# Kernel tuning notes

Hardware: AMD Instinct MI355X
Metric: run time of the kernel (lower is better)

The kernel has to match this reference:

```python
import jax, jax.numpy as jnp
import numpy as np

WS = 7           # window size
NH = 12          # num heads
EPS_ADA = 1e-6   # AdaLayerNorm eps
EPS_LN = 1e-5    # torch nn.LayerNorm default eps


def _rel_pos_index(ws):
    coords = np.stack(np.meshgrid(np.arange(ws), np.arange(ws), indexing='ij'))  # (2,ws,ws)
    flat = coords.reshape(2, -1)                      # (2, N)
    rel = flat[:, :, None] - flat[:, None, :]         # (2, N, N)
    rel = rel.transpose(1, 2, 0).astype(np.int64)     # (N, N, 2)
    rel[:, :, 0] += ws - 1
    rel[:, :, 1] += ws - 1
    rel[:, :, 0] *= 2 * ws - 1
    return jnp.asarray(rel.sum(-1))                   # (N, N) in [0, (2ws-1)^2)

REL_IDX = _rel_pos_index(WS)


def setup_inputs() -> dict:
    key = jax.random.key(0)
    ks = jax.random.split(key, 8)
    B, H, W, C, COND = 32, 56, 56, 384, 128
    L = H * W
    s = 0.02
    return {
        'x_tok': jax.random.normal(ks[0], (B, L, C), jnp.float32),
        'z_tok': jax.random.normal(ks[1], (B, L, C), jnp.float32),
        'cond': jax.random.normal(ks[2], (B, COND), jnp.float32),
        'gamma_x': jnp.ones((C,), jnp.float32),
        'beta_x': jnp.zeros((C,), jnp.float32),
        'mod_w': jax.random.normal(ks[3], (COND, 2 * C), jnp.float32) * s,
        'mod_b': jnp.zeros((2 * C,), jnp.float32),
        'gamma_z': jnp.ones((C,), jnp.float32),
        'beta_z': jnp.zeros((C,), jnp.float32),
        'rel_bias_table': jax.random.normal(ks[4], ((2 * WS - 1) ** 2, NH), jnp.float32) * s,
        'q_w': jax.random.normal(ks[5], (C, C), jnp.float32) * s,
        'q_b': jnp.zeros((C,), jnp.float32),
        'kv_w': jax.random.normal(ks[6], (C, 2 * C), jnp.float32) * s,
        'kv_b': jnp.zeros((2 * C,), jnp.float32),
        'proj_w': jax.random.normal(ks[7], (C, C), jnp.float32) * s,
        'proj_b': jnp.zeros((C,), jnp.float32),
        'H': H,
        'W': W,
    }


def reference(x_tok, z_tok, cond, gamma_x, beta_x, mod_w, mod_b,
              gamma_z, beta_z, rel_bias_table, q_w, q_b, kv_w, kv_b,
              proj_w, proj_b, H, W):
    B, L, C = x_tok.shape
    hd = C // NH
    N = WS * WS

    # AdaLayerNorm-Zero on x
    mu = x_tok.mean(-1, keepdims=True)
    var = ((x_tok - mu) ** 2).mean(-1, keepdims=True)
    x_hat = (x_tok - mu) * jax.lax.rsqrt(var + EPS_ADA)
    mod = (cond @ mod_w + mod_b).reshape(B, 2, C)
    d_gamma, d_beta = mod[:, 0], mod[:, 1]
    x = (gamma_x * (1.0 + d_gamma))[:, None, :] * x_hat + (beta_x + d_beta)[:, None, :]

    # LayerNorm on z
    mz = z_tok.mean(-1, keepdims=True)
    vz = ((z_tok - mz) ** 2).mean(-1, keepdims=True)
    z = (z_tok - mz) * jax.lax.rsqrt(vz + EPS_LN) * gamma_z + beta_z

    # window partition: (B,H,W,C) -> (B*nW, N, C)
    def part(t):
        t = t.reshape(B, H // WS, WS, W // WS, WS, C)
        return t.transpose(0, 1, 3, 2, 4, 5).reshape(-1, N, C)

    x_win = part(x.reshape(B, H, W, C))
    z_win = part(z.reshape(B, H, W, C))

    # cross window attention
    q = (x_win @ q_w + q_b).reshape(-1, N, NH, hd).transpose(0, 2, 1, 3)  # (Bw,H,N,d)
    kv = (z_win @ kv_w + kv_b).reshape(-1, N, 2, NH, hd)
    k = kv[:, :, 0].transpose(0, 2, 1, 3)
    v = kv[:, :, 1].transpose(0, 2, 1, 3)
    scale = hd ** -0.5
    attn = jnp.einsum('bhnd,bhmd->bhnm', q * scale, k)                    # (Bw,H,N,N)
    bias = rel_bias_table[REL_IDX.reshape(-1)].reshape(N, N, NH).transpose(2, 0, 1)
    attn = jax.nn.softmax(attn + bias[None], axis=-1)
    out = jnp.einsum('bhnm,bhmd->bhnd', attn, v).transpose(0, 2, 1, 3).reshape(-1, N, C)
    out = out @ proj_w + proj_b

    # window reverse: (B*nW, N, C) -> (B, L, C)
    fused = out.reshape(B, H // WS, W // WS, WS, WS, C)
    fused = fused.transpose(0, 1, 3, 2, 4, 5).reshape(B, L, C)

    return x_tok + fused
```

## Files before the change

kernel.cpp:

```cpp
#include <hip/hip_runtime.h>
#include <hip/hip_bf16.h>

typedef float f32x4 __attribute__((ext_vector_type(4)));
typedef short short8 __attribute__((ext_vector_type(8)));
typedef __hip_bfloat16 bf16;

constexpr int CDIM  = 384;
constexpr int LTOK  = 3136;
constexpr int NWIN  = 2048;
constexpr int MROWS = 100352;
constexpr int MPAD  = MROWS + 64;

__device__ __forceinline__ void gload_lds16(const void* g, void* l) {
  __builtin_amdgcn_global_load_lds(
      (const __attribute__((address_space(1))) void*)g,
      (__attribute__((address_space(3))) void*)l, 16, 0, 0);
}

__device__ __forceinline__ void row_to_bl(int r, int& b, int& l) {
  int w = r / 49, n = r % 49;
  b = w >> 6;
  int wrem = w & 63;
  int wy = wrem >> 3, wx = wrem & 7;
  int ny = n / 7, nx = n % 7;
  l = (wy * 7 + ny) * 56 + wx * 7 + nx;
}


__global__ __launch_bounds__(256) void mod_kernel(
    const float* __restrict__ cond, const float* __restrict__ mw,
    const float* __restrict__ mb, float* __restrict__ mod) {
  int idx = blockIdx.x * 256 + threadIdx.x;
  int b = idx / 768, j = idx % 768;
  float s = mb[j];
  const float* cr = cond + b * 128;
  #pragma unroll 4
  for (int k = 0; k < 128; k++) s += cr[k] * mw[(size_t)k * 768 + j];
  mod[idx] = s;
}

__global__ __launch_bounds__(256) void prep_wt(
    const float* __restrict__ qw, const float* __restrict__ kvw,
    const float* __restrict__ pw,
    bf16* __restrict__ wtq, bf16* __restrict__ wtkv, bf16* __restrict__ wtp) {
  int idx = blockIdx.x * 256 + threadIdx.x;
  if (idx < 147456) {
    int n = idx / 384, k = idx % 384;
    wtq[idx] = __float2bfloat16(qw[(size_t)k * 384 + n]);
  } else if (idx < 147456 + 294912) {
    int i = idx - 147456;
    int n = i / 384, k = i % 384;
    wtkv[i] = __float2bfloat16(kvw[(size_t)k * 768 + n]);
  } else {
    int i = idx - 442368;
    int n = i / 384, k = i % 384;
    wtp[i] = __float2bfloat16(pw[(size_t)k * 384 + n]);
  }
}

__global__ __launch_bounds__(256) void bias_kernel(
    const float* __restrict__ tab, float* __restrict__ bT) {
  int idx = blockIdx.x * 256 + threadIdx.x;
  int h = idx >> 12, rem = idx & 4095, m = rem >> 6, c = rem & 63;
  float v;
  if (c >= 49)      v = -1e30f;
  else if (m >= 49) v = 0.f;
  else {
    int yq = m / 7, xq = m % 7, yk = c / 7, xk = c % 7;
    v = tab[((yq - yk + 6) * 13 + (xq - xk + 6)) * 12 + h];
  }
  bT[idx] = v;
}


__global__ __launch_bounds__(256) void ln_kernel(
    const float* __restrict__ src, const float* __restrict__ gamma,
    const float* __restrict__ beta, const float* __restrict__ mod,
    float eps, bf16* __restrict__ dst) {
  int wid = threadIdx.x >> 6, lane = threadIdx.x & 63;
  int r = blockIdx.x * 4 + wid;
  int bb, ll; row_to_bl(r, bb, ll);
  const float* x = src + ((size_t)bb * LTOK + ll) * 384;
  float v[6]; float s = 0.f, s2 = 0.f;
  #pragma unroll
  for (int i = 0; i < 6; i++) {
    v[i] = x[lane + 64 * i];
    s += v[i]; s2 += v[i] * v[i];
  }
  #pragma unroll
  for (int d = 1; d < 64; d <<= 1) { s += __shfl_xor(s, d); s2 += __shfl_xor(s2, d); }
  float mu = s * (1.f / 384.f);
  float var = s2 * (1.f / 384.f) - mu * mu;
  float rstd = rsqrtf(var + eps);
  bf16* o = dst + (size_t)r * 384;
  if (mod != nullptr) {
    const float* mg = mod + bb * 768;
    #pragma unroll
    for (int i = 0; i < 6; i++) {
      int c = lane + 64 * i;
      float y = (gamma[c] * (1.f + mg[c])) * ((v[i] - mu) * rstd) + beta[c] + mg[384 + c];
      o[c] = __float2bfloat16(y);
    }
  } else {
    #pragma unroll
    for (int i = 0; i < 6; i++) {
      int c = lane + 64 * i;
      o[c] = __float2bfloat16((v[i] - mu) * rstd * gamma[c] + beta[c]);
    }
  }
}


template<int MODE>
__global__ __launch_bounds__(256) void gemm_kernel(
    const bf16* __restrict__ A, const bf16* __restrict__ WT,
    const float* __restrict__ bias, void* __restrict__ outp,
    const float* __restrict__ resid, float scale, int N) {
  __shared__ __align__(16) bf16 As[128 * 64];
  __shared__ __align__(16) bf16 Bs[128 * 64];
  const int bm = blockIdx.x * 128;
  const int bn = blockIdx.y * 128;
  const int t = threadIdx.x;
  const int wid = t >> 6, lane = t & 63;
  const int r16 = lane & 15, g = lane >> 4;
  const int wr = wid >> 1, wc = wid & 1;

  f32x4 acc[4][4] = {};

  for (int k0 = 0; k0 < 384; k0 += 64) {
    if (k0) __syncthreads();
    #pragma unroll
    for (int i = 0; i < 4; i++) {
      int c = wid * 256 + i * 64 + lane;
      int row = c >> 3, col8 = (c & 7) << 3;
      gload_lds16(A + (size_t)(bm + row) * 384 + k0 + col8,
                  (char*)As + (size_t)(wid * 256 + i * 64) * 16);
    }
    #pragma unroll
    for (int i = 0; i < 4; i++) {
      int c = wid * 256 + i * 64 + lane;
      int row = c >> 3, col8 = (c & 7) << 3;
      gload_lds16(WT + (size_t)(bn + row) * 384 + k0 + col8,
                  (char*)Bs + (size_t)(wid * 256 + i * 64) * 16);
    }
    __syncthreads();
    #pragma unroll
    for (int kk = 0; kk < 2; kk++) {
      short8 a[4], b[4];
      #pragma unroll
      for (int m = 0; m < 4; m++)
        a[m] = *(const short8*)((const char*)As + (wr * 64 + m * 16 + r16) * 128 + kk * 64 + g * 16);
      #pragma unroll
      for (int n = 0; n < 4; n++)
        b[n] = *(const short8*)((const char*)Bs + (wc * 64 + n * 16 + r16) * 128 + kk * 64 + g * 16);
      #pragma unroll
      for (int m = 0; m < 4; m++)
        #pragma unroll
        for (int n = 0; n < 4; n++)
          acc[m][n] = __builtin_amdgcn_mfma_f32_16x16x32_bf16(a[m], b[n], acc[m][n], 0, 0, 0);
    }
  }

  if (MODE == 0) {
    bf16* O = (bf16*)outp;
    #pragma unroll
    for (int n = 0; n < 4; n++) {
      int col = bn + wc * 64 + n * 16 + r16;
      float bc = bias[col];
      #pragma unroll
      for (int m = 0; m < 4; m++) {
        int row0 = bm + wr * 64 + m * 16 + g * 4;
        #pragma unroll
        for (int r = 0; r < 4; r++) {
          float v = (acc[m][n][r] + bc) * scale;
          O[(size_t)(row0 + r) * N + col] = __float2bfloat16(v);
        }
      }
    }
  } else {
    float* O = (float*)outp;
    #pragma unroll
    for (int m = 0; m < 4; m++) {
      #pragma unroll
      for (int r = 0; r < 4; r++) {
        int row = bm + wr * 64 + m * 16 + g * 4 + r;
        int bb, ll; row_to_bl(row, bb, ll);
        size_t base = ((size_t)bb * LTOK + ll) * 384;
        #pragma unroll
        for (int n = 0; n < 4; n++) {
          int col = bn + wc * 64 + n * 16 + r16;
          O[base + col] = resid[base + col] + acc[m][n][r] + bias[col];
        }
      }
    }
  }
}


__global__ __launch_bounds__(64) void attn_kernel(
    const bf16* __restrict__ q, const bf16* __restrict__ kv,
    const float* __restrict__ biasT, bf16* __restrict__ o) {
  __shared__ __align__(16) bf16 vt[32][72];
  __shared__ __align__(16) bf16 P[64][72];
  const int h = blockIdx.x, w = blockIdx.y;
  const int lane = threadIdx.x;
  const int r16 = lane & 15, g = lane >> 4;
  const size_t qbase = (size_t)w * 49 * 384 + h * 32;
  const size_t kvbase = (size_t)w * 49 * 768 + h * 32;

  for (int e = lane; e < 32 * 72; e += 64) ((bf16*)vt)[e] = __float2bfloat16(0.f);
  for (int e = lane; e < 49 * 32; e += 64) {
    int c = e >> 5, d = e & 31;
    vt[d][c] = kv[kvbase + (size_t)c * 768 + 384 + d];
  }

  short8 aq[4], bk[4];
  #pragma unroll
  for (int mi = 0; mi < 4; mi++)
    aq[mi] = *(const short8*)(q + qbase + (size_t)(mi * 16 + r16) * 384 + g * 8);
  #pragma unroll
  for (int ni = 0; ni < 4; ni++)
    bk[ni] = *(const short8*)(kv + kvbase + (size_t)(ni * 16 + r16) * 768 + g * 8);

  f32x4 zero = {0.f, 0.f, 0.f, 0.f};
  f32x4 S[4][4];
  #pragma unroll
  for (int mi = 0; mi < 4; mi++)
    #pragma unroll
    for (int ni = 0; ni < 4; ni++)
      S[mi][ni] = __builtin_amdgcn_mfma_f32_16x16x32_bf16(aq[mi], bk[ni], zero, 0, 0, 0);

  const float* bt = biasT + h * 4096;
  #pragma unroll
  for (int mi = 0; mi < 4; mi++) {
    #pragma unroll
    for (int r = 0; r < 4; r++) {
      int rowm = mi * 16 + g * 4 + r;
      float sv[4];
      #pragma unroll
      for (int ni = 0; ni < 4; ni++)
        sv[ni] = S[mi][ni][r] + bt[rowm * 64 + ni * 16 + r16];
      float mx = fmaxf(fmaxf(sv[0], sv[1]), fmaxf(sv[2], sv[3]));
      #pragma unroll
      for (int d = 1; d < 16; d <<= 1) mx = fmaxf(mx, __shfl_xor(mx, d));
      float sum = 0.f;
      #pragma unroll
      for (int ni = 0; ni < 4; ni++) { sv[ni] = __expf(sv[ni] - mx); sum += sv[ni]; }
      #pragma unroll
      for (int d = 1; d < 16; d <<= 1) sum += __shfl_xor(sum, d);
      float inv = __fdividef(1.f, sum);
      #pragma unroll
      for (int ni = 0; ni < 4; ni++)
        P[rowm][ni * 16 + r16] = __float2bfloat16(sv[ni] * inv);
    }
  }
  __syncthreads();

  f32x4 acc[4][2] = {};
  #pragma unroll
  for (int c0 = 0; c0 < 2; c0++) {
    short8 ap[4], bv[2];
    #pragma unroll
    for (int mi = 0; mi < 4; mi++)
      ap[mi] = *(const short8*)((const char*)&P[0][0] + (mi * 16 + r16) * 144 + c0 * 64 + g * 16);
    #pragma unroll
    for (int di = 0; di < 2; di++)
      bv[di] = *(const short8*)((const char*)&vt[0][0] + (di * 16 + r16) * 144 + c0 * 64 + g * 16);
    #pragma unroll
    for (int mi = 0; mi < 4; mi++)
      #pragma unroll
      for (int di = 0; di < 2; di++)
        acc[mi][di] = __builtin_amdgcn_mfma_f32_16x16x32_bf16(ap[mi], bv[di], acc[mi][di], 0, 0, 0);
  }

  #pragma unroll
  for (int mi = 0; mi < 4; mi++) {
    #pragma unroll
    for (int r = 0; r < 4; r++) {
      int m = mi * 16 + g * 4 + r;
      if (m < 49) {
        #pragma unroll
        for (int di = 0; di < 2; di++)
          o[(size_t)(w * 49 + m) * 384 + h * 32 + di * 16 + r16] =
              __float2bfloat16(acc[mi][di][r]);
      }
    }
  }
}


extern "C" void kernel_launch(void* const* d_in, const int* in_sizes, int n_in,
                              void* d_out, int out_size, void* d_ws, size_t ws_size,
                              hipStream_t stream) {
  (void)in_sizes; (void)n_in; (void)out_size; (void)ws_size;
  const float* x_tok   = (const float*)d_in[0];
  const float* z_tok   = (const float*)d_in[1];
  const float* cond    = (const float*)d_in[2];
  const float* gamma_x = (const float*)d_in[3];
  const float* beta_x  = (const float*)d_in[4];
  const float* mod_w   = (const float*)d_in[5];
  const float* mod_b   = (const float*)d_in[6];
  const float* gamma_z = (const float*)d_in[7];
  const float* beta_z  = (const float*)d_in[8];
  const float* rel_tab = (const float*)d_in[9];
  const float* q_b     = (const float*)d_in[11];
  const float* kv_b    = (const float*)d_in[13];
  const float* proj_b  = (const float*)d_in[15];
  const float* q_w     = (const float*)d_in[10];
  const float* kv_w    = (const float*)d_in[12];
  const float* proj_w  = (const float*)d_in[14];

  char* ws = (char*)d_ws;
  float* modbuf = (float*)(ws + 0);
  bf16*  wtq    = (bf16*)(ws + 98304);
  bf16*  wtkv   = (bf16*)(ws + 98304 + 294912);
  bf16*  wtp    = (bf16*)(ws + 98304 + 294912 + 589824);
  float* biasT  = (float*)(ws + 98304 + 294912 + 589824 + 294912);
  char*  R1     = ws + 1474560;
  char*  R2     = R1 + (size_t)MPAD * 384 * 2;
  char*  R3     = R2 + (size_t)MPAD * 384 * 2;

  hipMemsetAsync(R2 + (size_t)MROWS * 384 * 2, 0, 64 * 384 * 2, stream);
  hipMemsetAsync(R3 + (size_t)MROWS * 768 * 2, 0, 64 * 768 * 2, stream);

  mod_kernel <<<96,   256, 0, stream>>>(cond, mod_w, mod_b, modbuf);
  prep_wt    <<<2304, 256, 0, stream>>>(q_w, kv_w, proj_w, wtq, wtkv, wtp);
  bias_kernel<<<192,  256, 0, stream>>>(rel_tab, biasT);

  ln_kernel<<<25088, 256, 0, stream>>>(x_tok, gamma_x, beta_x, modbuf, 1e-6f, (bf16*)R1);
  gemm_kernel<0><<<dim3(784, 3), 256, 0, stream>>>(
      (const bf16*)R1, wtq, q_b, R2, nullptr, 0.17677669529663687f, 384);
  ln_kernel<<<25088, 256, 0, stream>>>(z_tok, gamma_z, beta_z, nullptr, 1e-5f, (bf16*)R1);
  gemm_kernel<0><<<dim3(784, 6), 256, 0, stream>>>(
      (const bf16*)R1, wtkv, kv_b, R3, nullptr, 1.0f, 768);
  attn_kernel<<<dim3(12, NWIN), 64, 0, stream>>>(
      (const bf16*)R2, (const bf16*)R3, biasT, (bf16*)R1);
  gemm_kernel<1><<<dim3(784, 3), 256, 0, stream>>>(
      (const bf16*)R1, wtp, proj_b, d_out, x_tok, 1.0f, 384);
}
```

Baseline: 611.2 us.

## Keep A tile in registers and stream pre-swizzled weight chunks per GEMM block

The GEMM is restructured so each block owns 128 rows across all output columns. The full K=384 A fragment stays in registers, and 64-column weight chunks are streamed into LDS from a pre-swizzled layout that prep_wt now writes. This removes the repeated A reloads across column tiles and the per-k-step syncs, at the cost of higher register pressure and serialized chunk loads with no double buffering. The LayerNorm kernel is also vectorized with float4 loads and 4-wide bf16 stores.

Measured after the change: 656.0 us. +7.3%, slower.

```diff
diff --git a/kernel.cpp b/kernel.cpp
--- a/kernel.cpp
+++ b/kernel.cpp
@@ -44,18 +44,14 @@
     const float* __restrict__ pw,
     bf16* __restrict__ wtq, bf16* __restrict__ wtkv, bf16* __restrict__ wtp) {
   int idx = blockIdx.x * 256 + threadIdx.x;
-  if (idx < 147456) {
-    int n = idx / 384, k = idx % 384;
-    wtq[idx] = __float2bfloat16(qw[(size_t)k * 384 + n]);
-  } else if (idx < 147456 + 294912) {
-    int i = idx - 147456;
-    int n = i / 384, k = i % 384;
-    wtkv[i] = __float2bfloat16(kvw[(size_t)k * 768 + n]);
-  } else {
-    int i = idx - 442368;
-    int n = i / 384, k = i % 384;
-    wtp[i] = __float2bfloat16(pw[(size_t)k * 384 + n]);
-  }
+  const float* src; bf16* dst; int i, Wn;
+  if (idx < 147456)      { i = idx;          src = qw;  dst = wtq;  Wn = 384; }
+  else if (idx < 442368) { i = idx - 147456; src = kvw; dst = wtkv; Wn = 768; }
+  else                   { i = idx - 442368; src = pw;  dst = wtp;  Wn = 384; }
+  int j = i & 7, n = (i >> 3) & 63, g = (i >> 9) & 3;
+  int kt = (i >> 11) % 12, chunk = i / 24576;
+  int k = kt * 32 + g * 8 + j, ng = chunk * 64 + n;
+  dst[i] = __float2bfloat16(src[(size_t)k * Wn + ng]);
 }
 
 __global__ __launch_bounds__(256) void bias_kernel(
@@ -73,6 +69,8 @@
 }
 
 
+struct alignas(8) B4 { bf16 h[4]; };
+
 __global__ __launch_bounds__(256) void ln_kernel(
     const float* __restrict__ src, const float* __restrict__ gamma,
     const float* __restrict__ beta, const float* __restrict__ mod,
@@ -80,116 +78,131 @@
   int wid = threadIdx.x >> 6, lane = threadIdx.x & 63;
   int r = blockIdx.x * 4 + wid;
   int bb, ll; row_to_bl(r, bb, ll);
-  const float* x = src + ((size_t)bb * LTOK + ll) * 384;
-  float v[6]; float s = 0.f, s2 = 0.f;
-  #pragma unroll
-  for (int i = 0; i < 6; i++) {
-    v[i] = x[lane + 64 * i];
-    s += v[i]; s2 += v[i] * v[i];
-  }
+  const f32x4* x4 = (const f32x4*)(src + ((size_t)bb * LTOK + ll) * 384);
+  f32x4 a = x4[lane];
+  f32x4 b = {0.f, 0.f, 0.f, 0.f};
+  if (lane < 32) b = x4[64 + lane];
+  float s  = a[0] + a[1] + a[2] + a[3] + b[0] + b[1] + b[2] + b[3];
+  float s2 = a[0]*a[0] + a[1]*a[1] + a[2]*a[2] + a[3]*a[3]
+           + b[0]*b[0] + b[1]*b[1] + b[2]*b[2] + b[3]*b[3];
   #pragma unroll
   for (int d = 1; d < 64; d <<= 1) { s += __shfl_xor(s, d); s2 += __shfl_xor(s2, d); }
   float mu = s * (1.f / 384.f);
   float var = s2 * (1.f / 384.f) - mu * mu;
   float rstd = rsqrtf(var + eps);
   bf16* o = dst + (size_t)r * 384;
+  const f32x4* g4 = (const f32x4*)gamma;
+  const f32x4* be4 = (const f32x4*)beta;
   if (mod != nullptr) {
-    const float* mg = mod + bb * 768;
-    #pragma unroll
-    for (int i = 0; i < 6; i++) {
-      int c = lane + 64 * i;
-      float y = (gamma[c] * (1.f + mg[c])) * ((v[i] - mu) * rstd) + beta[c] + mg[384 + c];
-      o[c] = __float2bfloat16(y);
+    const f32x4* mg4 = (const f32x4*)(mod + bb * 768);
+    const f32x4* mb4 = (const f32x4*)(mod + bb * 768 + 384);
+    {
+      f32x4 gg = g4[lane], bb2 = be4[lane], mg = mg4[lane], mb = mb4[lane];
+      B4 p;
+      #pragma unroll
+      for (int i = 0; i < 4; i++)
+        p.h[i] = __float2bfloat16((gg[i] * (1.f + mg[i])) * ((a[i] - mu) * rstd) + bb2[i] + mb[i]);
+      *((B4*)o + lane) = p;
+    }
+    if (lane < 32) {
+      f32x4 gg = g4[64 + lane], bb2 = be4[64 + lane], mg = mg4[64 + lane], mb = mb4[64 + lane];
+      B4 p;
+      #pragma unroll
+      for (int i = 0; i < 4; i++)
+        p.h[i] = __float2bfloat16((gg[i] * (1.f + mg[i])) * ((b[i] - mu) * rstd) + bb2[i] + mb[i]);
+      *((B4*)o + 64 + lane) = p;
     }
   } else {
-    #pragma unroll
-    for (int i = 0; i < 6; i++) {
-      int c = lane + 64 * i;
-      o[c] = __float2bfloat16((v[i] - mu) * rstd * gamma[c] + beta[c]);
+    {
+      f32x4 gg = g4[lane], bb2 = be4[lane];
+      B4 p;
+      #pragma unroll
+      for (int i = 0; i < 4; i++)
+        p.h[i] = __float2bfloat16((a[i] - mu) * rstd * gg[i] + bb2[i]);
+      *((B4*)o + lane) = p;
+    }
+    if (lane < 32) {
+      f32x4 gg = g4[64 + lane], bb2 = be4[64 + lane];
+      B4 p;
+      #pragma unroll
+      for (int i = 0; i < 4; i++)
+        p.h[i] = __float2bfloat16((b[i] - mu) * rstd * gg[i] + bb2[i]);
+      *((B4*)o + 64 + lane) = p;
     }
   }
 }
 
 
 template<int MODE>
-__global__ __launch_bounds__(256) void gemm_kernel(
-    const bf16* __restrict__ A, const bf16* __restrict__ WT,
+__global__ __launch_bounds__(256, 3) void gemm2(
+    const bf16* __restrict__ A, const bf16* __restrict__ WTt,
     const float* __restrict__ bias, void* __restrict__ outp,
     const float* __restrict__ resid, float scale, int N) {
-  __shared__ __align__(16) bf16 As[128 * 64];
-  __shared__ __align__(16) bf16 Bs[128 * 64];
-  const int bm = blockIdx.x * 128;
-  const int bn = blockIdx.y * 128;
+  __shared__ __align__(16) char Bs[49152];
   const int t = threadIdx.x;
   const int wid = t >> 6, lane = t & 63;
   const int r16 = lane & 15, g = lane >> 4;
-  const int wr = wid >> 1, wc = wid & 1;
-
-  f32x4 acc[4][4] = {};
-
-  for (int k0 = 0; k0 < 384; k0 += 64) {
-    if (k0) __syncthreads();
-    #pragma unroll
-    for (int i = 0; i < 4; i++) {
-      int c = wid * 256 + i * 64 + lane;
-      int row = c >> 3, col8 = (c & 7) << 3;
-      gload_lds16(A + (size_t)(bm + row) * 384 + k0 + col8,
-                  (char*)As + (size_t)(wid * 256 + i * 64) * 16);
-    }
-    #pragma unroll
-    for (int i = 0; i < 4; i++) {
-      int c = wid * 256 + i * 64 + lane;
-      int row = c >> 3, col8 = (c & 7) << 3;
-      gload_lds16(WT + (size_t)(bn + row) * 384 + k0 + col8,
-                  (char*)Bs + (size_t)(wid * 256 + i * 64) * 16);
-    }
+  const int wr0 = blockIdx.x * 128 + wid * 32;
+
+  short8 aF[2][12];
+  #pragma unroll
+  for (int m = 0; m < 2; m++)
+    #pragma unroll
+    for (int kt = 0; kt < 12; kt++)
+      aF[m][kt] = *(const short8*)(A + (size_t)(wr0 + m * 16 + r16) * 384 + kt * 32 + g * 8);
+
+  const int NCH = N >> 6;
+  auto stage = [&](int c) {
+    const char* srcp = (const char*)WTt + (size_t)c * 49152;
+    #pragma unroll
+    for (int i = 0; i < 12; i++)
+      gload_lds16(srcp + (i * 256 + t) * 16, Bs + (i * 256 + t) * 16);
+  };
+  stage(0);
+
+  for (int c = 0; c < NCH; c++) {
     __syncthreads();
-    #pragma unroll
-    for (int kk = 0; kk < 2; kk++) {
-      short8 a[4], b[4];
-      #pragma unroll
-      for (int m = 0; m < 4; m++)
-        a[m] = *(const short8*)((const char*)As + (wr * 64 + m * 16 + r16) * 128 + kk * 64 + g * 16);
-      #pragma unroll
-      for (int n = 0; n < 4; n++)
-        b[n] = *(const short8*)((const char*)Bs + (wc * 64 + n * 16 + r16) * 128 + kk * 64 + g * 16);
-      #pragma unroll
-      for (int m = 0; m < 4; m++)
+    f32x4 acc[2][4] = {};
+    #pragma unroll
+    for (int kt = 0; kt < 12; kt++) {
+      #pragma unroll
+      for (int ni = 0; ni < 4; ni++) {
+        short8 bF = *(const short8*)(Bs + kt * 4096 + g * 1024 + (ni * 16 + r16) * 16);
+        acc[0][ni] = __builtin_amdgcn_mfma_f32_16x16x32_bf16(aF[0][kt], bF, acc[0][ni], 0, 0, 0);
+        acc[1][ni] = __builtin_amdgcn_mfma_f32_16x16x32_bf16(aF[1][kt], bF, acc[1][ni], 0, 0, 0);
+      }
+    }
+    __syncthreads();
+    if (c + 1 < NCH) stage(c + 1);
+
+    if (MODE == 0) {
+      bf16* O = (bf16*)outp;
+      #pragma unroll
+      for (int ni = 0; ni < 4; ni++) {
+        int col = c * 64 + ni * 16 + r16;
+        float bc = bias[col];
         #pragma unroll
-        for (int n = 0; n < 4; n++)
-          acc[m][n] = __builtin_amdgcn_mfma_f32_16x16x32_bf16(a[m], b[n], acc[m][n], 0, 0, 0);
-    }
-  }
-
-  if (MODE == 0) {
-    bf16* O = (bf16*)outp;
-    #pragma unroll
-    for (int n = 0; n < 4; n++) {
-      int col = bn + wc * 64 + n * 16 + r16;
-      float bc = bias[col];
-      #pragma unroll
-      for (int m = 0; m < 4; m++) {
-        int row0 = bm + wr * 64 + m * 16 + g * 4;
-        #pragma unroll
-        for (int r = 0; r < 4; r++) {
-          float v = (acc[m][n][r] + bc) * scale;
-          O[(size_t)(row0 + r) * N + col] = __float2bfloat16(v);
+        for (int m = 0; m < 2; m++) {
+          int row0 = wr0 + m * 16 + g * 4;
+          #pragma unroll
+          for (int rr = 0; rr < 4; rr++)
+            O[(size_t)(row0 + rr) * N + col] = __float2bfloat16((acc[m][ni][rr] + bc) * scale);
         }
       }
-    }
-  } else {
-    float* O = (float*)outp;
-    #pragma unroll
-    for (int m = 0; m < 4; m++) {
-      #pragma unroll
-      for (int r = 0; r < 4; r++) {
-        int row = bm + wr * 64 + m * 16 + g * 4 + r;
-        int bb, ll; row_to_bl(row, bb, ll);
-        size_t base = ((size_t)bb * LTOK + ll) * 384;
+    } else {
+      float* O = (float*)outp;
+      #pragma unroll
+      for (int m = 0; m < 2; m++) {
         #pragma unroll
-        for (int n = 0; n < 4; n++) {
-          int col = bn + wc * 64 + n * 16 + r16;
-          O[base + col] = resid[base + col] + acc[m][n][r] + bias[col];
+        for (int rr = 0; rr < 4; rr++) {
+          int row = wr0 + m * 16 + g * 4 + rr;
+          int bb, ll; row_to_bl(row, bb, ll);
+          size_t base = ((size_t)bb * LTOK + ll) * 384;
+          #pragma unroll
+          for (int ni = 0; ni < 4; ni++) {
+            int col = c * 64 + ni * 16 + r16;
+            O[base + col] = resid[base + col] + acc[m][ni][rr] + bias[col];
+          }
         }
       }
     }
@@ -303,12 +316,12 @@
   const float* gamma_z = (const float*)d_in[7];
   const float* beta_z  = (const float*)d_in[8];
   const float* rel_tab = (const float*)d_in[9];
+  const float* q_w     = (const float*)d_in[10];
   const float* q_b     = (const float*)d_in[11];
+  const float* kv_w    = (const float*)d_in[12];
   const float* kv_b    = (const float*)d_in[13];
+  const float* proj_w  = (const float*)d_in[14];
   const float* proj_b  = (const float*)d_in[15];
-  const float* q_w     = (const float*)d_in[10];
-  const float* kv_w    = (const float*)d_in[12];
-  const float* proj_w  = (const float*)d_in[14];
 
   char* ws = (char*)d_ws;
   float* modbuf = (float*)(ws + 0);
@@ -328,13 +341,13 @@
   bias_kernel<<<192,  256, 0, stream>>>(rel_tab, biasT);
 
   ln_kernel<<<25088, 256, 0, stream>>>(x_tok, gamma_x, beta_x, modbuf, 1e-6f, (bf16*)R1);
-  gemm_kernel<0><<<dim3(784, 3), 256, 0, stream>>>(
+  gemm2<0><<<784, 256, 0, stream>>>(
       (const bf16*)R1, wtq, q_b, R2, nullptr, 0.17677669529663687f, 384);
   ln_kernel<<<25088, 256, 0, stream>>>(z_tok, gamma_z, beta_z, nullptr, 1e-5f, (bf16*)R1);
-  gemm_kernel<0><<<dim3(784, 6), 256, 0, stream>>>(
+  gemm2<0><<<784, 256, 0, stream>>>(
       (const bf16*)R1, wtkv, kv_b, R3, nullptr, 1.0f, 768);
   attn_kernel<<<dim3(12, NWIN), 64, 0, stream>>>(
       (const bf16*)R2, (const bf16*)R3, biasT, (bf16*)R1);
-  gemm_kernel<1><<<dim3(784, 3), 256, 0, stream>>>(
+  gemm2<1><<<784, 256, 0, stream>>>(
       (const bf16*)R1, wtp, proj_b, d_out, x_tok, 1.0f, 384);
 }
```
